# Kernel optimization log

Hardware: AMD Instinct MI355X
Metric: run time of the kernel (lower is better)

The kernel has to match this reference:

```python
import jax, jax.numpy as jnp
import numpy as np

LN = 8   # local_numbers
R = 2    # upscale_factor


def pixelshuffle(x, r):
    N, C, H, W = x.shape
    x = x.reshape(N, C // (r * r), r, r, H, W).transpose(0, 1, 4, 2, 5, 3)
    return x.reshape(N, C // (r * r), H * r, W * r)


def pixelunshuffle(x, r):
    N, C, H, W = x.shape
    x = x.reshape(N, C, H // r, r, W // r, r).transpose(0, 1, 3, 5, 2, 4)
    return x.reshape(N, C * r * r, H // r, W // r)


def layernorm(x, g, b):
    mu = jnp.mean(x, -1, keepdims=True)
    v = jnp.mean((x - mu) ** 2, -1, keepdims=True)
    return (x - mu) * jax.lax.rsqrt(v + 1e-5) * g + b


def mamba_fwd(x, in_w, conv_w, conv_b, xproj_w, dt_w, dt_b, A_log, Dp, out_w):
    # x: [N, L, d_model]
    d_inner = conv_w.shape[0]
    d_conv = conv_w.shape[1]
    d_state = A_log.shape[1]
    dt_rank = dt_w.shape[1]
    xz = x @ in_w.T                       # [N, L, 2*d_inner]
    xi, z = xz[..., :d_inner], xz[..., d_inner:]
    # causal depthwise conv1d
    xt = jnp.swapaxes(xi, 1, 2)           # [N, d_inner, L]
    xc = jax.lax.conv_general_dilated(
        xt, conv_w[:, None, :], (1,), [(d_conv - 1, 0)],
        feature_group_count=d_inner, dimension_numbers=('NCH', 'OIH', 'NCH'))
    xc = jax.nn.silu(jnp.swapaxes(xc + conv_b[None, :, None], 1, 2))  # [N, L, d_inner]
    x_dbl = xc @ xproj_w.T                # [N, L, dt_rank + 2*d_state]
    dt = x_dbl[..., :dt_rank]
    Bm = x_dbl[..., dt_rank:dt_rank + d_state]
    Cm = x_dbl[..., dt_rank + d_state:]
    dt = jax.nn.softplus(dt @ dt_w.T + dt_b)      # [N, L, d_inner]
    A = -jnp.exp(A_log)                            # [d_inner, d_state]
    a = jnp.exp(dt[..., None] * A)                 # [N, L, d_inner, d_state]
    b = dt[..., None] * Bm[:, :, None, :] * xc[..., None]

    def comb(l, r):
        return (l[0] * r[0], r[0] * l[1] + r[1])

    _, h = jax.lax.associative_scan(comb, (a, b), axis=1)
    y = jnp.einsum('nlds,nls->nld', h, Cm) + Dp * xc
    y = y * jax.nn.silu(z)
    return y @ out_w.T


def _make_mamba(key, d_model, d_state, d_conv, expand):
    di = expand * d_model
    dtr = max(1, (d_model + 15) // 16)
    k = jax.random.split(key, 5)
    s = 0.05
    return {
        'in_w': s * jax.random.normal(k[0], (2 * di, d_model), jnp.float32),
        'conv_w': s * jax.random.normal(k[1], (di, d_conv), jnp.float32),
        'conv_b': jnp.zeros((di,), jnp.float32),
        'xproj_w': s * jax.random.normal(k[2], (dtr + 2 * d_state, di), jnp.float32),
        'dt_w': s * jax.random.normal(k[3], (di, dtr), jnp.float32),
        'dt_b': jnp.full((di,), -4.6, jnp.float32),  # softplus(-4.6) ~ 0.01
        'A_log': jnp.log(jnp.broadcast_to(jnp.arange(1, d_state + 1, dtype=jnp.float32), (di, d_state))),
        'D': jnp.ones((di,), jnp.float32),
        'out_w': s * jax.random.normal(k[4], (d_model, di), jnp.float32),
    }


def setup_inputs() -> dict:
    key = jax.random.key(0)
    ks = jax.random.split(key, 6)
    B, C, H, W = 2, 64, 128, 128
    dm = 16  # d_model for all three modes (C//4 == H//8 == W//8 == 16)
    inp = {'x': jax.random.normal(ks[0], (B, C, H, W), jnp.float32)}
    inp['gt1'] = 0.02 * jax.random.normal(ks[1], (1, 1, dm), jnp.float32)
    inp['gt2'] = 0.02 * jax.random.normal(ks[2], (1, 1, dm), jnp.float32)
    inp['ln1_g'] = jnp.ones((dm,), jnp.float32)
    inp['ln1_b'] = jnp.zeros((dm,), jnp.float32)
    inp['ln2_g'] = jnp.ones((dm,), jnp.float32)
    inp['ln2_b'] = jnp.zeros((dm,), jnp.float32)
    for i, pfx in enumerate(['m1_', 'm2_']):
        p = _make_mamba(ks[3 + i], dm, 16, 4, 2)
        for k_, v in p.items():
            inp[pfx + k_] = v
    return inp


def reference(x, gt1, gt2, ln1_g, ln1_b, ln2_g, ln2_b,
              m1_in_w, m1_conv_w, m1_conv_b, m1_xproj_w, m1_dt_w, m1_dt_b, m1_A_log, m1_D, m1_out_w,
              m2_in_w, m2_conv_w, m2_conv_b, m2_xproj_w, m2_dt_w, m2_dt_b, m2_A_log, m2_D, m2_out_w):
    B, C, H, W = x.shape
    ch, cw = H // LN, W // LN
    nc = LN * LN
    # unfold into local chunks: [B*nc, C, ch, cw]
    xu = x.reshape(B, C, LN, ch, LN, cw).transpose(0, 2, 4, 1, 3, 5).reshape(B * nc, C, ch, cw)
    m1 = (m1_in_w, m1_conv_w, m1_conv_b, m1_xproj_w, m1_dt_w, m1_dt_b, m1_A_log, m1_D, m1_out_w)
    m2 = (m2_in_w, m2_conv_w, m2_conv_b, m2_xproj_w, m2_dt_w, m2_dt_b, m2_A_log, m2_D, m2_out_w)
    outs = []
    for mode in range(3):
        if mode == 0:
            xm = pixelshuffle(xu, R).reshape(B, nc, C // (R * R), ch * R, cw * R)
        else:
            x5 = xu.reshape(B, nc, C, ch, cw)
            xm = x5.transpose(0, 1, 3, 2, 4) if mode == 1 else x5.transpose(0, 1, 4, 2, 3)
        d, Hc, Wc = xm.shape[2], xm.shape[3], xm.shape[4]
        L = Hc * Wc
        xf = jnp.swapaxes(xm.reshape(B * nc, d, L), 1, 2)   # [B*nc, L, d]
        g = gt1 if mode == 0 else gt2
        gt = jnp.broadcast_to(g, (B * nc, g.shape[1], g.shape[2]))
        xf = jnp.concatenate([gt, xf], axis=1)
        if mode == 0:
            y = mamba_fwd(layernorm(xf, ln1_g, ln1_b), *m1)
        else:
            y = mamba_fwd(layernorm(xf, ln2_g, ln2_b), *m2)
        y = y[:, -L:, :]
        out5 = jnp.swapaxes(y, 1, 2).reshape(B, nc, d, Hc, Wc)
        if mode == 1:
            out5 = out5.transpose(0, 1, 3, 2, 4)
        elif mode == 2:
            out5 = out5.transpose(0, 1, 3, 4, 2)
        out4 = out5.reshape(B * nc, out5.shape[2], out5.shape[3], out5.shape[4])
        if mode == 0:
            out4 = pixelunshuffle(out4, R)
        Co, Ho, Wo = out4.shape[1], out4.shape[2], out4.shape[3]
        # replicate torch's view->permute->reshape reassembly exactly
        out = out4.reshape(B, nc, Co, Ho, Wo).transpose(0, 2, 1, 3, 4).reshape(B, Co, LN * Ho, LN * Wo)
        outs.append(out)
    return (outs[0] + outs[1] + outs[2]) / 3.0
```

## Files before the change

### kernel.cpp

```cpp
#include <hip/hip_runtime.h>
#include <cmath>

namespace {

constexpr int XC = 64, XH = 128, XW = 128;
constexpr int NSEQ = 128;
constexpr int TLEN = 1025;
constexpr int LSEQ = 1024;
constexpr int TT = 96;
constexpr int NT = 11;

struct MP {
    const float *in_w, *conv_w, *conv_b, *xproj_w, *dt_w, *dt_b, *A_log, *D, *out_w;
};

__device__ __forceinline__ int xidx(int b, int c, int h, int w) {
    return ((b * XC + c) * XH + h) * XW + w;
}
__device__ __forceinline__ int oidx(int b, int cube, int c, int i, int j) {
    int h = cube * 2 + (i >> 3);
    int w = ((i & 7) << 4) | j;
    return xidx(b, c, h, w);
}
__device__ __forceinline__ float siluf(float v) { return v / (1.0f + __expf(-v)); }
__device__ __forceinline__ float softplusf(float v) {
    return v > 20.0f ? v : log1pf(__expf(v));
}

template <int MODE>
__device__ __forceinline__ float gather_val(const float* __restrict__ x,
                                            const float* __restrict__ s_gt,
                                            int t, int k, int b, int bi, int bj) {
    if (t == 0) return s_gt[k];
    int l = t - 1;
    if (MODE == 0) {
        int i2 = l >> 5, j2 = l & 31;
        int h = bi * 16 + (i2 >> 1), w = bj * 16 + (j2 >> 1);
        int coff = ((i2 & 1) << 1) | (j2 & 1);
        return x[xidx(b, k * 4 + coff, h, w)];
    } else if (MODE == 1) {
        int c = l >> 4, j = l & 15;
        return x[xidx(b, c, bi * 16 + k, bj * 16 + j)];
    } else {
        int c = l >> 4, i = l & 15;
        return x[xidx(b, c, bi * 16 + i, bj * 16 + k)];
    }
}
__device__ __forceinline__ float gather_rt(int mode, const float* __restrict__ x,
                                           const float* __restrict__ s_gt,
                                           int t, int k, int b, int bi, int bj) {
    if (mode == 0) return gather_val<0>(x, s_gt, t, k, b, bi, bj);
    if (mode == 1) return gather_val<1>(x, s_gt, t, k, b, bi, bj);
    return gather_val<2>(x, s_gt, t, k, b, bi, bj);
}

template <int MODE_C>
__global__ __launch_bounds__(256) void k_p1(
    const float* __restrict__ x,
    const float* __restrict__ gt1, const float* __restrict__ gt2,
    const float* __restrict__ ln1g, const float* __restrict__ ln1b,
    const float* __restrict__ ln2g, const float* __restrict__ ln2b,
    MP P0, MP P1, int mode_base,
    float* __restrict__ VB0, float* __restrict__ SC0, size_t arena)
{
    const int mode = (MODE_C >= 0) ? MODE_C : (mode_base + (int)blockIdx.y);
    const MP P = (mode == 0) ? P0 : P1;
    const float* gt  = (mode == 0) ? gt1 : gt2;
    const float* lng = (mode == 0) ? ln1g : ln2g;
    const float* lnb = (mode == 0) ? ln1b : ln2b;
    float* VB = VB0 + (size_t)blockIdx.y * arena;
    float* sc = SC0 + (size_t)blockIdx.y * arena;

    const int n = blockIdx.x / NT, tile = blockIdx.x % NT;
    const int t0 = tile * TT;
    const int ntk = min(TT, TLEN - t0);
    const int nth = ntk + 3;
    const int b = n >> 6, cube = n & 63, bi = cube >> 3, bj = cube & 7;
    const int tid = threadIdx.x;

    __shared__ __align__(16) float s_pool[TT * 37];
    float (*s_v)[17]  = (float(*)[17])s_pool;
    float (*s_xc)[37] = (float(*)[37])s_pool;
    __shared__ __align__(16) float s_xi[TT + 3][36];
    __shared__ __align__(16) float s_wT[16][32];
    __shared__ __align__(16) float s_xpT[32][36];
    __shared__ float s_xp0[32];
    __shared__ float s_cw[128], s_cb[32], s_dw[32], s_db[32];
    __shared__ float s_g[16], s_bb[16], s_gt[16];
    __shared__ float s_dt0[TT];

    for (int i = tid; i < 32 * 16; i += 256) s_wT[i & 15][i >> 4] = P.in_w[i];
    for (int i = tid; i < 33 * 32; i += 256) {
        int r = i >> 5, cc = i & 31;
        float v = P.xproj_w[i];
        if (r == 0) s_xp0[cc] = v;
        else s_xpT[cc][r - 1] = v;
    }
    if (tid < 128) s_cw[tid] = P.conv_w[tid];
    if (tid < 32) { s_cb[tid] = P.conv_b[tid]; s_dw[tid] = P.dt_w[tid]; s_db[tid] = P.dt_b[tid]; }
    if (tid < 16) { s_g[tid] = lng[tid]; s_bb[tid] = lnb[tid]; s_gt[tid] = gt[tid]; }
    __syncthreads();

    for (int it = tid; it < nth * 16; it += 256) {
        int tl = it >> 4, k = it & 15;
        int t = t0 - 3 + tl;
        float v;
        if (t < 0) v = 0.f;
        else if (MODE_C >= 0) v = gather_val<(MODE_C >= 0 ? MODE_C : 0)>(x, s_gt, t, k, b, bi, bj);
        else v = gather_rt(mode, x, s_gt, t, k, b, bi, bj);
        s_v[tl][k] = v;
    }
    __syncthreads();

    for (int tl = tid; tl < nth; tl += 256) {
        int t = t0 - 3 + tl;
        if (t < 0) continue;
        float v[16], mu = 0.f;
#pragma unroll
        for (int k = 0; k < 16; k++) { v[k] = s_v[tl][k]; mu += v[k]; }
        mu *= (1.f / 16.f);
        float var = 0.f;
#pragma unroll
        for (int k = 0; k < 16; k++) { float d = v[k] - mu; var += d * d; }
        float inv = rsqrtf(var * (1.f / 16.f) + 1e-5f);
#pragma unroll
        for (int k = 0; k < 16; k++) s_v[tl][k] = (v[k] - mu) * inv * s_g[k] + s_bb[k];
    }
    __syncthreads();

    {
        float* vb = VB + ((size_t)n * TLEN + t0) * 16;
        for (int it = tid; it < ntk * 16; it += 256) {
            int j = it >> 4, k = it & 15;
            vb[it] = s_v[j + 3][k];
        }
        const int ntt = (nth + 3) >> 2;
        for (int tl0 = tid; tl0 < ntt * 8; tl0 += 256) {
            int tt = tl0 >> 3, og = tl0 & 7;
            int oc = og * 4;
            float acc[4][4] = {{0.f}};
#pragma unroll
            for (int k = 0; k < 16; k++) {
                float4 wv = *(const float4*)&s_wT[k][oc];
                float a0 = s_v[4 * tt + 0][k];
                float a1 = s_v[4 * tt + 1][k];
                float a2 = s_v[4 * tt + 2][k];
                float a3 = s_v[4 * tt + 3][k];
                acc[0][0] += a0 * wv.x; acc[0][1] += a0 * wv.y; acc[0][2] += a0 * wv.z; acc[0][3] += a0 * wv.w;
                acc[1][0] += a1 * wv.x; acc[1][1] += a1 * wv.y; acc[1][2] += a1 * wv.z; acc[1][3] += a1 * wv.w;
                acc[2][0] += a2 * wv.x; acc[2][1] += a2 * wv.y; acc[2][2] += a2 * wv.z; acc[2][3] += a2 * wv.w;
                acc[3][0] += a3 * wv.x; acc[3][1] += a3 * wv.y; acc[3][2] += a3 * wv.z; acc[3][3] += a3 * wv.w;
            }
#pragma unroll
            for (int i = 0; i < 4; i++) {
                int tl = 4 * tt + i;
                if (tl >= nth) break;
                *(float4*)&s_xi[tl][oc] =
                    make_float4(acc[i][0], acc[i][1], acc[i][2], acc[i][3]);
            }
        }
    }
    __syncthreads();

    {
        int cc = tid & 31, jg = tid >> 5;
        float c0 = s_cw[cc * 4 + 0], c1 = s_cw[cc * 4 + 1];
        float c2 = s_cw[cc * 4 + 2], c3 = s_cw[cc * 4 + 3];
        float cb = s_cb[cc];
        float* scb = sc + ((size_t)n * TLEN + t0) * 96;
        for (int j = jg; j < ntk; j += 8) {
            float acc = 0.f;
            acc += c0 * s_xi[j + 0][cc];
            acc += c1 * s_xi[j + 1][cc];
            acc += c2 * s_xi[j + 2][cc];
            acc += c3 * s_xi[j + 3][cc];
            float v = siluf(acc + cb);
            s_xc[j][cc] = v;
            scb[j * 96 + cc] = v;
        }
    }
    __syncthreads();

    {
        int qt = tid & 7, tt = tid >> 3;
        if (4 * tt < ntk) {
            float acc[4][4] = {{0.f}};
#pragma unroll
            for (int cc = 0; cc < 32; cc++) {
                float4 wv = *(const float4*)&s_xpT[cc][4 * qt];
                float a0 = s_xc[4 * tt + 0][cc];
                float a1 = s_xc[4 * tt + 1][cc];
                float a2 = s_xc[4 * tt + 2][cc];
                float a3 = s_xc[4 * tt + 3][cc];
                acc[0][0] += a0 * wv.x; acc[0][1] += a0 * wv.y; acc[0][2] += a0 * wv.z; acc[0][3] += a0 * wv.w;
                acc[1][0] += a1 * wv.x; acc[1][1] += a1 * wv.y; acc[1][2] += a1 * wv.z; acc[1][3] += a1 * wv.w;
                acc[2][0] += a2 * wv.x; acc[2][1] += a2 * wv.y; acc[2][2] += a2 * wv.z; acc[2][3] += a2 * wv.w;
                acc[3][0] += a3 * wv.x; acc[3][1] += a3 * wv.y; acc[3][2] += a3 * wv.z; acc[3][3] += a3 * wv.w;
            }
#pragma unroll
            for (int i = 0; i < 4; i++) {
                int j = 4 * tt + i;
                if (j < ntk)
                    *(float4*)&sc[((size_t)n * TLEN + t0 + j) * 96 + 64 + 4 * qt] =
                        make_float4(acc[i][0], acc[i][1], acc[i][2], acc[i][3]);
            }
        }
        if (tid < ntk) {
            float acc = 0.f;
#pragma unroll
            for (int cc = 0; cc < 32; cc++) acc += s_xc[tid][cc] * s_xp0[cc];
            s_dt0[tid] = acc;
        }
    }
    __syncthreads();

    {
        float* scb = sc + ((size_t)n * TLEN + t0) * 96;
        for (int it = tid; it < ntk * 32; it += 256) {
            int j = it >> 5, d = it & 31;
            scb[j * 96 + 32 + d] = softplusf(s_dt0[j] * s_dw[d] + s_db[d]);
        }
    }
}

template <int MODE_C, int CHUNKT, int NCHT>
__global__ __launch_bounds__(128) void k_scan1(
    const float* __restrict__ SC0, MP P0, MP P1, int mode_base,
    float* __restrict__ PS0, float* __restrict__ FS0, size_t arena)
{
    const int mode = (MODE_C >= 0) ? MODE_C : (mode_base + (int)blockIdx.y);
    const float* A_log = (mode == 0) ? P0.A_log : P1.A_log;
    const float* sc = SC0 + (size_t)blockIdx.y * arena;
    float* Psum = PS0 + (size_t)blockIdx.y * arena;
    float* Fsum = FS0 + (size_t)blockIdx.y * arena;

    int n = blockIdx.x / NCHT;
    int c = blockIdx.x % NCHT;
    int t0 = c * CHUNKT;
    int nt = min(CHUNKT, TLEN - t0);
    __shared__ __align__(16) float s_sc[CHUNKT * 80];
    const float* src = sc + ((size_t)n * TLEN + t0) * 96;
    for (int i = threadIdx.x; i < nt * 20; i += 128) {
        int row = i / 20, q = i - row * 20;
        ((float4*)s_sc)[row * 20 + q] = *(const float4*)&src[row * 96 + q * 4];
    }
    int tid = threadIdx.x, d = tid >> 2, sg = tid & 3;
    float4 Av = *(const float4*)&A_log[d * 16 + sg * 4];
    float A0 = -__expf(Av.x), A1 = -__expf(Av.y), A2 = -__expf(Av.z), A3 = -__expf(Av.w);
    __syncthreads();
    float h0 = 0.f, h1 = 0.f, h2 = 0.f, h3 = 0.f;
    float P0v = 1.f, P1v = 1.f, P2v = 1.f, P3v = 1.f;
    for (int t = 0; t < nt; t++) {
        const float* p = s_sc + t * 80;
        float dt = p[32 + d], xc = p[d];
        float4 Bv = *(const float4*)&p[64 + sg * 4];
        float a0 = __expf(dt * A0); h0 = a0 * h0 + dt * Bv.x * xc; P0v *= a0;
        float a1 = __expf(dt * A1); h1 = a1 * h1 + dt * Bv.y * xc; P1v *= a1;
        float a2 = __expf(dt * A2); h2 = a2 * h2 + dt * Bv.z * xc; P2v *= a2;
        float a3 = __expf(dt * A3); h3 = a3 * h3 + dt * Bv.w * xc; P3v *= a3;
    }
    size_t base = ((size_t)n * NCHT + c) * 512 + d * 16 + sg * 4;
    *(float4*)&Psum[base] = make_float4(P0v, P1v, P2v, P3v);
    *(float4*)&Fsum[base] = make_float4(h0, h1, h2, h3);
}

template <int NCHT>
__global__ __launch_bounds__(512) void k_comb(
    const float* __restrict__ PS0, const float* __restrict__ FS0,
    float* __restrict__ HI0, size_t arena)
{
    const float* Psum = PS0 + (size_t)blockIdx.y * arena;
    const float* Fsum = FS0 + (size_t)blockIdx.y * arena;
    float* Hin = HI0 + (size_t)blockIdx.y * arena;
    int n = blockIdx.x, tid = threadIdx.x;
    const float* pb = Psum + (size_t)n * NCHT * 512;
    const float* fb = Fsum + (size_t)n * NCHT * 512;
    float* hb = Hin + (size_t)n * NCHT * 512;
    float H = 0.f;
#pragma unroll
    for (int c = 0; c < NCHT; c++) {
        float P = pb[(size_t)c * 512 + tid];
        float F = fb[(size_t)c * 512 + tid];
        hb[(size_t)c * 512 + tid] = H;
        H = F + P * H;
    }
}

template <int MODE_C, int CHUNKT, int NCHT>
__global__ __launch_bounds__(128) void k_scan2(
    float* __restrict__ SC0, MP P0, MP P1, int mode_base,
    const float* __restrict__ HI0, size_t arena)
{
    const int mode = (MODE_C >= 0) ? MODE_C : (mode_base + (int)blockIdx.y);
    const float* A_log = (mode == 0) ? P0.A_log : P1.A_log;
    const float* Dp = (mode == 0) ? P0.D : P1.D;
    float* sc = SC0 + (size_t)blockIdx.y * arena;
    const float* Hin = HI0 + (size_t)blockIdx.y * arena;

    int n = blockIdx.x / NCHT;
    int c = blockIdx.x % NCHT;
    int t0 = c * CHUNKT;
    int nt = min(CHUNKT, TLEN - t0);
    __shared__ __align__(16) float s_sc[CHUNKT * 96];
    const float* src = sc + ((size_t)n * TLEN + t0) * 96;
    int nv4 = nt * 24;
    for (int i = threadIdx.x; i < nv4; i += 128)
        ((float4*)s_sc)[i] = ((const float4*)src)[i];
    int tid = threadIdx.x, d = tid >> 2, sg = tid & 3;
    float4 Av = *(const float4*)&A_log[d * 16 + sg * 4];
    float A0 = -__expf(Av.x), A1 = -__expf(Av.y), A2 = -__expf(Av.z), A3 = -__expf(Av.w);
    float Dd = Dp[d];
    float4 Hv = *(const float4*)&Hin[((size_t)n * NCHT + c) * 512 + d * 16 + sg * 4];
    float h0 = Hv.x, h1 = Hv.y, h2 = Hv.z, h3 = Hv.w;
    __syncthreads();
    for (int t = 0; t < nt; t++) {
        float* p = s_sc + t * 96;
        float dt = p[32 + d], xc = p[d];
        float4 Bv = *(const float4*)&p[64 + sg * 4];
        float4 Cv = *(const float4*)&p[80 + sg * 4];
        float a0 = __expf(dt * A0); h0 = a0 * h0 + dt * Bv.x * xc;
        float a1 = __expf(dt * A1); h1 = a1 * h1 + dt * Bv.y * xc;
        float a2 = __expf(dt * A2); h2 = a2 * h2 + dt * Bv.z * xc;
        float a3 = __expf(dt * A3); h3 = a3 * h3 + dt * Bv.w * xc;
        float pp = h0 * Cv.x + h1 * Cv.y + h2 * Cv.z + h3 * Cv.w;
        pp += __shfl_xor(pp, 1);
        pp += __shfl_xor(pp, 2);
        if (sg == 0) p[d] = pp + Dd * xc;
    }
    __syncthreads();
    float* yb = sc + ((size_t)n * TLEN + t0) * 96;
    for (int i = threadIdx.x; i < nt * 8; i += 128) {
        int j = i >> 3, q = i & 7;
        *(float4*)&yb[j * 96 + q * 4] = *(const float4*)&s_sc[j * 96 + q * 4];
    }
}

template <int MODE>
__global__ void k_p3(const float* __restrict__ ysc, const float* __restrict__ VB,
                     const float* __restrict__ in_w,
                     const float* __restrict__ out_w,
                     float* __restrict__ out)
{
    __shared__ float s_w[16 * 32];
    __shared__ float s_wz[16][32];
    for (int i = threadIdx.x; i < 512; i += blockDim.x) {
        s_w[i] = out_w[i];
        int oc = i >> 4, k = i & 15;
        s_wz[k][oc] = in_w[(32 + oc) * 16 + k];
    }
    __syncthreads();
    int tid = blockIdx.x * blockDim.x + threadIdx.x;
    if (tid >= NSEQ * LSEQ) return;
    int n = tid >> 10, l = tid & 1023, t = l + 1;
    const float* y = ysc + ((size_t)n * TLEN + t) * 96;
    const float* vv = VB + ((size_t)n * TLEN + t) * 16;
    float v[16];
#pragma unroll
    for (int k = 0; k < 16; k++) v[k] = vv[k];
    float yv[32];
#pragma unroll
    for (int c = 0; c < 32; c++) {
        float z = 0.f;
#pragma unroll
        for (int k = 0; k < 16; k++) z += v[k] * s_wz[k][c];
        yv[c] = y[c] * siluf(z);
    }
    float o[16];
#pragma unroll
    for (int j = 0; j < 16; j++) {
        float acc = 0.f;
#pragma unroll
        for (int c = 0; c < 32; c++) acc += yv[c] * s_w[j * 32 + c];
        o[j] = acc * (1.0f / 3.0f);
    }
    int b = n >> 6, cube = n & 63;
    if (MODE == 0) {
        int i2 = l >> 5, j2 = l & 31;
        int io = i2 >> 1, jo = j2 >> 1;
        int coff = ((i2 & 1) << 1) | (j2 & 1);
#pragma unroll
        for (int j = 0; j < 16; j++) out[oidx(b, cube, j * 4 + coff, io, jo)] = o[j];
    } else if (MODE == 1) {
        int c = l >> 4, jj = l & 15;
#pragma unroll
        for (int j = 0; j < 16; j++) out[oidx(b, cube, c, j, jj)] += o[j];
    } else {
        int c = l >> 4, ii = l & 15;
#pragma unroll
        for (int j = 0; j < 16; j++) out[oidx(b, cube, c, ii, j)] += o[j];
    }
}

}

extern "C" void kernel_launch(void* const* d_in, const int* in_sizes, int n_in,
                              void* d_out, int out_size, void* d_ws, size_t ws_size,
                              hipStream_t stream) {
    const float* x   = (const float*)d_in[0];
    const float* gt1 = (const float*)d_in[1];
    const float* gt2 = (const float*)d_in[2];
    const float* ln1g = (const float*)d_in[3];
    const float* ln1b = (const float*)d_in[4];
    const float* ln2g = (const float*)d_in[5];
    const float* ln2b = (const float*)d_in[6];
    MP P[2];
    for (int mi = 0; mi < 2; mi++) {
        P[mi].in_w   = (const float*)d_in[7 + mi * 9 + 0];
        P[mi].conv_w = (const float*)d_in[7 + mi * 9 + 1];
        P[mi].conv_b = (const float*)d_in[7 + mi * 9 + 2];
        P[mi].xproj_w= (const float*)d_in[7 + mi * 9 + 3];
        P[mi].dt_w   = (const float*)d_in[7 + mi * 9 + 4];
        P[mi].dt_b   = (const float*)d_in[7 + mi * 9 + 5];
        P[mi].A_log  = (const float*)d_in[7 + mi * 9 + 6];
        P[mi].D      = (const float*)d_in[7 + mi * 9 + 7];
        P[mi].out_w  = (const float*)d_in[7 + mi * 9 + 8];
    }
    float* out = (float*)d_out;

    const size_t VBs = (size_t)NSEQ * TLEN * 16;
    const size_t SCs = (size_t)NSEQ * TLEN * 96;
    const size_t PS16 = (size_t)NSEQ * 16 * 512;
    const size_t PS32 = (size_t)NSEQ * 32 * 512;
    const size_t arena16 = VBs + SCs + 3 * PS16;
    const size_t arena32 = VBs + SCs + 3 * PS32;

    float* A0 = (float*)d_ws;
    dim3 b256(256), b128(128), b512(512);
    dim3 grd3((NSEQ * LSEQ + 255) / 256);

    const bool fits3_32 = ws_size >= 3 * arena32 * sizeof(float);
    const bool fits3_16 = ws_size >= 3 * arena16 * sizeof(float);
    const bool fits2_16 = ws_size >= 2 * arena16 * sizeof(float);

    if (fits3_32) {
        const size_t arena = arena32;
        auto VB = [&](int y) { return A0 + (size_t)y * arena; };
        auto SC = [&](int y) { return A0 + (size_t)y * arena + VBs; };
        auto PS = [&](int y) { return A0 + (size_t)y * arena + VBs + SCs; };
        auto FS = [&](int y) { return PS(y) + PS32; };
        auto HI = [&](int y) { return FS(y) + PS32; };
        k_p1<-1><<<dim3(NSEQ * NT, 3), b256, 0, stream>>>(
            x, gt1, gt2, ln1g, ln1b, ln2g, ln2b, P[0], P[1], 0, VB(0), SC(0), arena);
        k_scan1<-1, 33, 32><<<dim3(NSEQ * 32, 3), b128, 0, stream>>>(
            SC(0), P[0], P[1], 0, PS(0), FS(0), arena);
        k_comb<32><<<dim3(NSEQ, 3), b512, 0, stream>>>(PS(0), FS(0), HI(0), arena);
        k_scan2<-1, 33, 32><<<dim3(NSEQ * 32, 3), b128, 0, stream>>>(
            SC(0), P[0], P[1], 0, HI(0), arena);
        k_p3<0><<<grd3, b256, 0, stream>>>(SC(0), VB(0), P[0].in_w, P[0].out_w, out);
        k_p3<1><<<grd3, b256, 0, stream>>>(SC(1), VB(1), P[1].in_w, P[1].out_w, out);
        k_p3<2><<<grd3, b256, 0, stream>>>(SC(2), VB(2), P[1].in_w, P[1].out_w, out);
    } else if (fits3_16) {
        const size_t arena = arena16;
        auto VB = [&](int y) { return A0 + (size_t)y * arena; };
        auto SC = [&](int y) { return A0 + (size_t)y * arena + VBs; };
        auto PS = [&](int y) { return A0 + (size_t)y * arena + VBs + SCs; };
        auto FS = [&](int y) { return PS(y) + PS16; };
        auto HI = [&](int y) { return FS(y) + PS16; };
        k_p1<-1><<<dim3(NSEQ * NT, 3), b256, 0, stream>>>(
            x, gt1, gt2, ln1g, ln1b, ln2g, ln2b, P[0], P[1], 0, VB(0), SC(0), arena);
        k_scan1<-1, 65, 16><<<dim3(NSEQ * 16, 3), b128, 0, stream>>>(
            SC(0), P[0], P[1], 0, PS(0), FS(0), arena);
        k_comb<16><<<dim3(NSEQ, 3), b512, 0, stream>>>(PS(0), FS(0), HI(0), arena);
        k_scan2<-1, 65, 16><<<dim3(NSEQ * 16, 3), b128, 0, stream>>>(
            SC(0), P[0], P[1], 0, HI(0), arena);
        k_p3<0><<<grd3, b256, 0, stream>>>(SC(0), VB(0), P[0].in_w, P[0].out_w, out);
        k_p3<1><<<grd3, b256, 0, stream>>>(SC(1), VB(1), P[1].in_w, P[1].out_w, out);
        k_p3<2><<<grd3, b256, 0, stream>>>(SC(2), VB(2), P[1].in_w, P[1].out_w, out);
    } else if (fits2_16) {
        const size_t arena = arena16;
        auto VB = [&](int y) { return A0 + (size_t)y * arena; };
        auto SC = [&](int y) { return A0 + (size_t)y * arena + VBs; };
        auto PS = [&](int y) { return A0 + (size_t)y * arena + VBs + SCs; };
        auto FS = [&](int y) { return PS(y) + PS16; };
        auto HI = [&](int y) { return FS(y) + PS16; };
        k_p1<0><<<dim3(NSEQ * NT, 1), b256, 0, stream>>>(
            x, gt1, gt2, ln1g, ln1b, ln2g, ln2b, P[0], P[1], 0, VB(0), SC(0), arena);
        k_scan1<0, 65, 16><<<dim3(NSEQ * 16, 1), b128, 0, stream>>>(
            SC(0), P[0], P[1], 0, PS(0), FS(0), arena);
        k_comb<16><<<dim3(NSEQ, 1), b512, 0, stream>>>(PS(0), FS(0), HI(0), arena);
        k_scan2<0, 65, 16><<<dim3(NSEQ * 16, 1), b128, 0, stream>>>(
            SC(0), P[0], P[1], 0, HI(0), arena);
        k_p3<0><<<grd3, b256, 0, stream>>>(SC(0), VB(0), P[0].in_w, P[0].out_w, out);
        k_p1<-1><<<dim3(NSEQ * NT, 2), b256, 0, stream>>>(
            x, gt1, gt2, ln1g, ln1b, ln2g, ln2b, P[0], P[1], 1, VB(0), SC(0), arena);
        k_scan1<-1, 65, 16><<<dim3(NSEQ * 16, 2), b128, 0, stream>>>(
            SC(0), P[0], P[1], 1, PS(0), FS(0), arena);
        k_comb<16><<<dim3(NSEQ, 2), b512, 0, stream>>>(PS(0), FS(0), HI(0), arena);
        k_scan2<-1, 65, 16><<<dim3(NSEQ * 16, 2), b128, 0, stream>>>(
            SC(0), P[0], P[1], 1, HI(0), arena);
        k_p3<1><<<grd3, b256, 0, stream>>>(SC(0), VB(0), P[1].in_w, P[1].out_w, out);
        k_p3<2><<<grd3, b256, 0, stream>>>(SC(1), VB(1), P[1].in_w, P[1].out_w, out);
    } else {
        const size_t arena = arena16;
        auto VB = [&](int y) { return A0 + (size_t)y * arena; };
        auto SC = [&](int y) { return A0 + (size_t)y * arena + VBs; };
        auto PS = [&](int y) { return A0 + (size_t)y * arena + VBs + SCs; };
        auto FS = [&](int y) { return PS(y) + PS16; };
        auto HI = [&](int y) { return FS(y) + PS16; };
        for (int mode = 0; mode < 3; mode++) {
            if (mode == 0)
                k_p1<0><<<dim3(NSEQ * NT, 1), b256, 0, stream>>>(
                    x, gt1, gt2, ln1g, ln1b, ln2g, ln2b, P[0], P[1], 0, VB(0), SC(0), arena);
            else if (mode == 1)
                k_p1<1><<<dim3(NSEQ * NT, 1), b256, 0, stream>>>(
                    x, gt1, gt2, ln1g, ln1b, ln2g, ln2b, P[0], P[1], 0, VB(0), SC(0), arena);
            else
                k_p1<2><<<dim3(NSEQ * NT, 1), b256, 0, stream>>>(
                    x, gt1, gt2, ln1g, ln1b, ln2g, ln2b, P[0], P[1], 0, VB(0), SC(0), arena);
            if (mode == 0)
                k_scan1<0, 65, 16><<<dim3(NSEQ * 16, 1), b128, 0, stream>>>(SC(0), P[0], P[1], 0, PS(0), FS(0), arena);
            else if (mode == 1)
                k_scan1<1, 65, 16><<<dim3(NSEQ * 16, 1), b128, 0, stream>>>(SC(0), P[0], P[1], 0, PS(0), FS(0), arena);
            else
                k_scan1<2, 65, 16><<<dim3(NSEQ * 16, 1), b128, 0, stream>>>(SC(0), P[0], P[1], 0, PS(0), FS(0), arena);
            k_comb<16><<<dim3(NSEQ, 1), b512, 0, stream>>>(PS(0), FS(0), HI(0), arena);
            if (mode == 0)
                k_scan2<0, 65, 16><<<dim3(NSEQ * 16, 1), b128, 0, stream>>>(SC(0), P[0], P[1], 0, HI(0), arena);
            else if (mode == 1)
                k_scan2<1, 65, 16><<<dim3(NSEQ * 16, 1), b128, 0, stream>>>(SC(0), P[0], P[1], 0, HI(0), arena);
            else
                k_scan2<2, 65, 16><<<dim3(NSEQ * 16, 1), b128, 0, stream>>>(SC(0), P[0], P[1], 0, HI(0), arena);
            if (mode == 0)      k_p3<0><<<grd3, b256, 0, stream>>>(SC(0), VB(0), P[0].in_w, P[0].out_w, out);
            else if (mode == 1) k_p3<1><<<grd3, b256, 0, stream>>>(SC(0), VB(0), P[1].in_w, P[1].out_w, out);
            else                k_p3<2><<<grd3, b256, 0, stream>>>(SC(0), VB(0), P[1].in_w, P[1].out_w, out);
        }
    }
}
```

Measured before the change: 291.9 us.

## Fuse silu(z) gating into scan2 and merge three output projections into one kernel

Moves the z-branch projection and silu gating from the output kernel into the second scan kernel, where the chunk's y values are already in shared memory, so the gated y is written back once. Replaces the three per-mode output-projection kernels with a single kernel that computes each output element from all three modes and writes it once, instead of three read-modify-write passes over the output. The fused output kernel reads mode-0 y rows straight from global memory with a scattered pattern, and scan2 now needs extra shared memory for the gating weights.

New measurement: 328.2 us. 1.12x slower.

```diff
diff --git a/kernel.cpp b/kernel.cpp
--- a/kernel.cpp
+++ b/kernel.cpp
@@ -288,13 +288,16 @@
 
 template <int MODE_C, int CHUNKT, int NCHT>
 __global__ __launch_bounds__(128) void k_scan2(
-    float* __restrict__ SC0, MP P0, MP P1, int mode_base,
+    float* __restrict__ SC0, const float* __restrict__ VB0,
+    MP P0, MP P1, int mode_base,
     const float* __restrict__ HI0, size_t arena)
 {
     const int mode = (MODE_C >= 0) ? MODE_C : (mode_base + (int)blockIdx.y);
-    const float* A_log = (mode == 0) ? P0.A_log : P1.A_log;
-    const float* Dp = (mode == 0) ? P0.D : P1.D;
+    const MP P = (mode == 0) ? P0 : P1;
+    const float* A_log = P.A_log;
+    const float* Dp = P.D;
     float* sc = SC0 + (size_t)blockIdx.y * arena;
+    const float* VB = VB0 + (size_t)blockIdx.y * arena;
     const float* Hin = HI0 + (size_t)blockIdx.y * arena;
 
     int n = blockIdx.x / NCHT;
@@ -302,10 +305,21 @@
     int t0 = c * CHUNKT;
     int nt = min(CHUNKT, TLEN - t0);
     __shared__ __align__(16) float s_sc[CHUNKT * 96];
+    __shared__ __align__(16) float s_val[CHUNKT][17];
+    __shared__ float s_wz[16][32];
     const float* src = sc + ((size_t)n * TLEN + t0) * 96;
     int nv4 = nt * 24;
     for (int i = threadIdx.x; i < nv4; i += 128)
         ((float4*)s_sc)[i] = ((const float4*)src)[i];
+    {
+        const float* vbp = VB + ((size_t)n * TLEN + t0) * 16;
+        for (int i = threadIdx.x; i < nt * 16; i += 128)
+            s_val[i >> 4][i & 15] = vbp[i];
+        for (int i = threadIdx.x; i < 512; i += 128) {
+            int cc = i >> 4, k = i & 15;
+            s_wz[k][cc] = P.in_w[(32 + cc) * 16 + k];
+        }
+    }
     int tid = threadIdx.x, d = tid >> 2, sg = tid & 3;
     float4 Av = *(const float4*)&A_log[d * 16 + sg * 4];
     float A0 = -__expf(Av.x), A1 = -__expf(Av.y), A2 = -__expf(Av.z), A3 = -__expf(Av.w);
@@ -329,42 +343,81 @@
     }
     __syncthreads();
     float* yb = sc + ((size_t)n * TLEN + t0) * 96;
-    for (int i = threadIdx.x; i < nt * 8; i += 128) {
-        int j = i >> 3, q = i & 7;
-        *(float4*)&yb[j * 96 + q * 4] = *(const float4*)&s_sc[j * 96 + q * 4];
-    }
+    for (int i = threadIdx.x; i < nt * 32; i += 128) {
+        int j = i >> 5, cc = i & 31;
+        float z = 0.f;
+#pragma unroll
+        for (int k = 0; k < 16; k++) z += s_val[j][k] * s_wz[k][cc];
+        yb[j * 96 + cc] = s_sc[j * 96 + cc] * siluf(z);
+    }
+}
+
+__global__ __launch_bounds__(256) void k_p3f(
+    const float* __restrict__ SC0,
+    const float* __restrict__ w0, const float* __restrict__ w12,
+    float* __restrict__ out, size_t arena)
+{
+    int bid = blockIdx.x;
+    int co = bid & 63, cube = (bid >> 6) & 63, b = bid >> 12;
+    int tid = threadIdx.x, i = tid >> 4, j = tid & 15;
+    int n = (b << 6) | cube;
+
+    __shared__ float s_w0[512], s_w12[512];
+    __shared__ __align__(16) float s_gy1[16][36], s_gy2[16][36];
+    const float* sc1 = SC0 + arena;
+    const float* sc2 = SC0 + 2 * arena;
+    for (int q = tid; q < 512; q += 256) { s_w0[q] = w0[q]; s_w12[q] = w12[q]; }
+    {
+        size_t rbase = ((size_t)n * TLEN + co * 16 + 1) * 96;
+        for (int q = tid; q < 16 * 8; q += 256) {
+            int r = q >> 3, f4 = q & 7;
+            *(float4*)&s_gy1[r][f4 * 4] = *(const float4*)&sc1[rbase + r * 96 + f4 * 4];
+            *(float4*)&s_gy2[r][f4 * 4] = *(const float4*)&sc2[rbase + r * 96 + f4 * 4];
+        }
+    }
+    __syncthreads();
+
+    int coff = co & 3, oj = co >> 2;
+    int l0 = (2 * i + (coff >> 1)) * 32 + 2 * j + (coff & 1);
+    const float* y0 = SC0 + ((size_t)n * TLEN + l0 + 1) * 96;
+    float o;
+    {
+        float acc = 0.f;
+#pragma unroll
+        for (int cc = 0; cc < 32; cc++) acc += y0[cc] * s_w0[oj * 32 + cc];
+        o = acc * (1.0f / 3.0f);
+    }
+    {
+        float acc = 0.f;
+#pragma unroll
+        for (int cc = 0; cc < 32; cc++) acc += s_gy1[j][cc] * s_w12[i * 32 + cc];
+        o += acc * (1.0f / 3.0f);
+    }
+    {
+        float acc = 0.f;
+#pragma unroll
+        for (int cc = 0; cc < 32; cc++) acc += s_gy2[i][cc] * s_w12[j * 32 + cc];
+        o += acc * (1.0f / 3.0f);
+    }
+    int h = cube * 2 + (i >> 3), w = ((i & 7) << 4) | j;
+    out[xidx(b, co, h, w)] = o;
 }
 
 template <int MODE>
-__global__ void k_p3(const float* __restrict__ ysc, const float* __restrict__ VB,
-                     const float* __restrict__ in_w,
-                     const float* __restrict__ out_w,
-                     float* __restrict__ out)
+__global__ void k_p3m(const float* __restrict__ ysc,
+                      const float* __restrict__ out_w,
+                      float* __restrict__ out)
 {
     __shared__ float s_w[16 * 32];
-    __shared__ float s_wz[16][32];
-    for (int i = threadIdx.x; i < 512; i += blockDim.x) {
-        s_w[i] = out_w[i];
-        int oc = i >> 4, k = i & 15;
-        s_wz[k][oc] = in_w[(32 + oc) * 16 + k];
-    }
+    for (int i = threadIdx.x; i < 512; i += blockDim.x) s_w[i] = out_w[i];
     __syncthreads();
     int tid = blockIdx.x * blockDim.x + threadIdx.x;
     if (tid >= NSEQ * LSEQ) return;
     int n = tid >> 10, l = tid & 1023, t = l + 1;
     const float* y = ysc + ((size_t)n * TLEN + t) * 96;
-    const float* vv = VB + ((size_t)n * TLEN + t) * 16;
-    float v[16];
-#pragma unroll
-    for (int k = 0; k < 16; k++) v[k] = vv[k];
     float yv[32];
 #pragma unroll
-    for (int c = 0; c < 32; c++) {
-        float z = 0.f;
-#pragma unroll
-        for (int k = 0; k < 16; k++) z += v[k] * s_wz[k][c];
-        yv[c] = y[c] * siluf(z);
-    }
+    for (int c = 0; c < 32; c++) yv[c] = y[c];
     float o[16];
 #pragma unroll
     for (int j = 0; j < 16; j++) {
@@ -445,10 +498,8 @@
             SC(0), P[0], P[1], 0, PS(0), FS(0), arena);
         k_comb<32><<<dim3(NSEQ, 3), b512, 0, stream>>>(PS(0), FS(0), HI(0), arena);
         k_scan2<-1, 33, 32><<<dim3(NSEQ * 32, 3), b128, 0, stream>>>(
-            SC(0), P[0], P[1], 0, HI(0), arena);
-        k_p3<0><<<grd3, b256, 0, stream>>>(SC(0), VB(0), P[0].in_w, P[0].out_w, out);
-        k_p3<1><<<grd3, b256, 0, stream>>>(SC(1), VB(1), P[1].in_w, P[1].out_w, out);
-        k_p3<2><<<grd3, b256, 0, stream>>>(SC(2), VB(2), P[1].in_w, P[1].out_w, out);
+            SC(0), VB(0), P[0], P[1], 0, HI(0), arena);
+        k_p3f<<<dim3(NSEQ * 64), b256, 0, stream>>>(SC(0), P[0].out_w, P[1].out_w, out, arena);
     } else if (fits3_16) {
         const size_t arena = arena16;
         auto VB = [&](int y) { return A0 + (size_t)y * arena; };
@@ -462,10 +513,8 @@
             SC(0), P[0], P[1], 0, PS(0), FS(0), arena);
         k_comb<16><<<dim3(NSEQ, 3), b512, 0, stream>>>(PS(0), FS(0), HI(0), arena);
         k_scan2<-1, 65, 16><<<dim3(NSEQ * 16, 3), b128, 0, stream>>>(
-            SC(0), P[0], P[1], 0, HI(0), arena);
-        k_p3<0><<<grd3, b256, 0, stream>>>(SC(0), VB(0), P[0].in_w, P[0].out_w, out);
-        k_p3<1><<<grd3, b256, 0, stream>>>(SC(1), VB(1), P[1].in_w, P[1].out_w, out);
-        k_p3<2><<<grd3, b256, 0, stream>>>(SC(2), VB(2), P[1].in_w, P[1].out_w, out);
+            SC(0), VB(0), P[0], P[1], 0, HI(0), arena);
+        k_p3f<<<dim3(NSEQ * 64), b256, 0, stream>>>(SC(0), P[0].out_w, P[1].out_w, out, arena);
     } else if (fits2_16) {
         const size_t arena = arena16;
         auto VB = [&](int y) { return A0 + (size_t)y * arena; };
@@ -479,17 +528,17 @@
             SC(0), P[0], P[1], 0, PS(0), FS(0), arena);
         k_comb<16><<<dim3(NSEQ, 1), b512, 0, stream>>>(PS(0), FS(0), HI(0), arena);
         k_scan2<0, 65, 16><<<dim3(NSEQ * 16, 1), b128, 0, stream>>>(
-            SC(0), P[0], P[1], 0, HI(0), arena);
-        k_p3<0><<<grd3, b256, 0, stream>>>(SC(0), VB(0), P[0].in_w, P[0].out_w, out);
+            SC(0), VB(0), P[0], P[1], 0, HI(0), arena);
+        k_p3m<0><<<grd3, b256, 0, stream>>>(SC(0), P[0].out_w, out);
         k_p1<-1><<<dim3(NSEQ * NT, 2), b256, 0, stream>>>(
             x, gt1, gt2, ln1g, ln1b, ln2g, ln2b, P[0], P[1], 1, VB(0), SC(0), arena);
         k_scan1<-1, 65, 16><<<dim3(NSEQ * 16, 2), b128, 0, stream>>>(
             SC(0), P[0], P[1], 1, PS(0), FS(0), arena);
         k_comb<16><<<dim3(NSEQ, 2), b512, 0, stream>>>(PS(0), FS(0), HI(0), arena);
         k_scan2<-1, 65, 16><<<dim3(NSEQ * 16, 2), b128, 0, stream>>>(
-            SC(0), P[0], P[1], 1, HI(0), arena);
-        k_p3<1><<<grd3, b256, 0, stream>>>(SC(0), VB(0), P[1].in_w, P[1].out_w, out);
-        k_p3<2><<<grd3, b256, 0, stream>>>(SC(1), VB(1), P[1].in_w, P[1].out_w, out);
+            SC(0), VB(0), P[0], P[1], 1, HI(0), arena);
+        k_p3m<1><<<grd3, b256, 0, stream>>>(SC(0), P[1].out_w, out);
+        k_p3m<2><<<grd3, b256, 0, stream>>>(SC(1), P[1].out_w, out);
     } else {
         const size_t arena = arena16;
         auto VB = [&](int y) { return A0 + (size_t)y * arena; };
@@ -515,14 +564,14 @@
                 k_scan1<2, 65, 16><<<dim3(NSEQ * 16, 1), b128, 0, stream>>>(SC(0), P[0], P[1], 0, PS(0), FS(0), arena);
             k_comb<16><<<dim3(NSEQ, 1), b512, 0, stream>>>(PS(0), FS(0), HI(0), arena);
             if (mode == 0)
-                k_scan2<0, 65, 16><<<dim3(NSEQ * 16, 1), b128, 0, stream>>>(SC(0), P[0], P[1], 0, HI(0), arena);
+                k_scan2<0, 65, 16><<<dim3(NSEQ * 16, 1), b128, 0, stream>>>(SC(0), VB(0), P[0], P[1], 0, HI(0), arena);
             else if (mode == 1)
-                k_scan2<1, 65, 16><<<dim3(NSEQ * 16, 1), b128, 0, stream>>>(SC(0), P[0], P[1], 0, HI(0), arena);
+                k_scan2<1, 65, 16><<<dim3(NSEQ * 16, 1), b128, 0, stream>>>(SC(0), VB(0), P[0], P[1], 0, HI(0), arena);
             else
-                k_scan2<2, 65, 16><<<dim3(NSEQ * 16, 1), b128, 0, stream>>>(SC(0), P[0], P[1], 0, HI(0), arena);
-            if (mode == 0)      k_p3<0><<<grd3, b256, 0, stream>>>(SC(0), VB(0), P[0].in_w, P[0].out_w, out);
-            else if (mode == 1) k_p3<1><<<grd3, b256, 0, stream>>>(SC(0), VB(0), P[1].in_w, P[1].out_w, out);
-            else                k_p3<2><<<grd3, b256, 0, stream>>>(SC(0), VB(0), P[1].in_w, P[1].out_w, out);
-        }
-    }
-}
+                k_scan2<2, 65, 16><<<dim3(NSEQ * 16, 1), b128, 0, stream>>>(SC(0), VB(0), P[0], P[1], 0, HI(0), arena);
+            if (mode == 0)      k_p3m<0><<<grd3, b256, 0, stream>>>(SC(0), P[0].out_w, out);
+            else if (mode == 1) k_p3m<1><<<grd3, b256, 0, stream>>>(SC(0), P[1].out_w, out);
+            else                k_p3m<2><<<grd3, b256, 0, stream>>>(SC(0), P[1].out_w, out);
+        }
+    }
+}
```
